# Optimization experiments

Measured on AMD Instinct MI355X. Metric: run time of the kernel, lower is better.

The kernel has to match this reference:

```python
import jax, jax.numpy as jnp
import numpy as np

B, S, E, H, D = 4, 2048, 1024, 16, 64


def setup_inputs() -> dict:
    key = jax.random.key(0)
    ks = jax.random.split(key, 10)
    s_in = 1.0 / np.sqrt(E)
    s_out = 1.0 / np.sqrt(H * D)
    return {
        "x": jax.random.normal(ks[0], (B, S, E), dtype=jnp.float32),
        "wq": jax.random.uniform(ks[1], (H, E, D), jnp.float32, -s_in, s_in),
        "bq": jax.random.uniform(ks[2], (H, D), jnp.float32, -s_in, s_in),
        "wk": jax.random.uniform(ks[3], (H, E, D), jnp.float32, -s_in, s_in),
        "bk": jax.random.uniform(ks[4], (H, D), jnp.float32, -s_in, s_in),
        "wv": jax.random.uniform(ks[5], (H, E, D), jnp.float32, -s_in, s_in),
        "bv": jax.random.uniform(ks[6], (H, D), jnp.float32, -s_in, s_in),
        "wo": jax.random.uniform(ks[7], (H * D, E), jnp.float32, -s_out, s_out),
        "bo": jax.random.uniform(ks[8], (E,), jnp.float32, -s_out, s_out),
    }


def reference(x, wq, bq, wk, bk, wv, bv, wo, bo):
    # Batched equivalent of the per-head Python loop: project all heads at once.
    q = jnp.einsum("bse,hed->bhsd", x, wq) + bq[None, :, None, :]
    k = jnp.einsum("bse,hed->bhsd", x, wk) + bk[None, :, None, :]
    v = jnp.einsum("bse,hed->bhsd", x, wv) + bv[None, :, None, :]
    scale = 1.0 / jnp.sqrt(jnp.asarray(D, dtype=x.dtype))
    scores = jnp.einsum("bhsd,bhtd->bhst", q, k) * scale  # [B,H,S,S]
    causal = jnp.tril(jnp.ones((S, S), dtype=bool))
    scores = jnp.where(causal[None, None], scores, jnp.asarray(-jnp.inf, x.dtype))
    p = jax.nn.softmax(scores, axis=-1)
    o = jnp.einsum("bhst,bhtd->bhsd", p, v)
    # concat heads along last dim (head order matches the torch cat order)
    o = jnp.transpose(o, (0, 2, 1, 3)).reshape(B, S, H * D)
    y = o @ wo + bo  # output projection; dropout is identity in eval
    return y
```

## Files before the change

### kernel.cpp

```cpp
#include <hip/hip_runtime.h>
#include <math.h>

#define B_ 4
#define S_ 2048
#define E_ 1024
#define H_ 16
#define D_ 64

using f32x4 = __attribute__((ext_vector_type(4))) float;
using s16x8 = __attribute__((ext_vector_type(8))) short;

__device__ __forceinline__ unsigned short f2bf(float f) {
    unsigned int u = __float_as_uint(f);
    u = (u + 0x7FFFu + ((u >> 16) & 1u)) >> 16;
    return (unsigned short)u;
}

__device__ __forceinline__ void load_lds16(const void* g, void* l) {
    __builtin_amdgcn_global_load_lds(
        (const __attribute__((address_space(1))) void*)g,
        (__attribute__((address_space(3))) void*)l, 16, 0, 0);
}

#define QSCALE 0.18033688011112042f

__global__ __launch_bounds__(256)
void cast_x(const float* __restrict__ in, unsigned short* __restrict__ out)
{
    const size_t idx = (size_t)blockIdx.x * 2048 + threadIdx.x * 8;
    const float4 v0 = *(const float4*)&in[idx];
    const float4 v1 = *(const float4*)&in[idx + 4];
    uint4 p;
    p.x = (unsigned)f2bf(v0.x) | ((unsigned)f2bf(v0.y) << 16);
    p.y = (unsigned)f2bf(v0.z) | ((unsigned)f2bf(v0.w) << 16);
    p.z = (unsigned)f2bf(v1.x) | ((unsigned)f2bf(v1.y) << 16);
    p.w = (unsigned)f2bf(v1.z) | ((unsigned)f2bf(v1.w) << 16);
    *(uint4*)&out[idx] = p;
}

__global__ __launch_bounds__(256)
void transpose_w(const float* __restrict__ wq, const float* __restrict__ wk,
                 const float* __restrict__ wv, const float* __restrict__ wo,
                 unsigned short* __restrict__ Wqkvt, unsigned short* __restrict__ Wot)
{
    __shared__ float T[64][68];
    const int z = blockIdx.z;
    const float* in;
    unsigned short* out;
    int inStride, r0, c0;
    if (z < 48) {
        if (blockIdx.y != 0) return;
        const int t = z >> 4, h = z & 15;
        const float* W = (t == 0) ? wq : ((t == 1) ? wk : wv);
        in = W + (size_t)h * (E_ * D_);
        inStride = 64;
        out = Wqkvt + (size_t)(t * 1024 + h * 64) * 1024;
        r0 = blockIdx.x * 64; c0 = 0;
    } else {
        in = wo; inStride = 1024;
        out = Wot;
        r0 = blockIdx.x * 64; c0 = blockIdx.y * 64;
    }
    const int tid = threadIdx.x;
    #pragma unroll
    for (int i = 0; i < 4; ++i) {
        const int e = tid + i * 256;
        const int row = e >> 4, c4 = e & 15;
        const float4 v = *(const float4*)&in[(size_t)(r0 + row) * inStride + c0 + c4 * 4];
        T[row][c4 * 4 + 0] = v.x; T[row][c4 * 4 + 1] = v.y;
        T[row][c4 * 4 + 2] = v.z; T[row][c4 * 4 + 3] = v.w;
    }
    __syncthreads();
    #pragma unroll
    for (int i = 0; i < 2; ++i) {
        const int e = tid + i * 256;
        const int c = e >> 3, ch = e & 7;
        unsigned short h8[8];
        #pragma unroll
        for (int j = 0; j < 8; ++j) h8[j] = f2bf(T[ch * 8 + j][c]);
        uint4 p;
        p.x = (unsigned)h8[0] | ((unsigned)h8[1] << 16);
        p.y = (unsigned)h8[2] | ((unsigned)h8[3] << 16);
        p.z = (unsigned)h8[4] | ((unsigned)h8[5] << 16);
        p.w = (unsigned)h8[6] | ((unsigned)h8[7] << 16);
        *(uint4*)&out[(size_t)(c0 + c) * 1024 + r0 + ch * 8] = p;
    }
}

template<int MODE>
__global__ __launch_bounds__(256)
void gemm_mfma(const unsigned short* __restrict__ A,
               const unsigned short* __restrict__ Bt,
               const float* __restrict__ bq, const float* __restrict__ bk,
               const float* __restrict__ bv, const float* __restrict__ bo,
               unsigned short* __restrict__ Qb, unsigned short* __restrict__ Kb,
               unsigned short* __restrict__ Vt, float* __restrict__ Cout)
{
    __shared__ short As[128 * 64];
    __shared__ short Bs[128 * 64];

    const int tid  = threadIdx.x;
    const int w    = tid >> 6, lane = tid & 63;
    const int g    = lane >> 4, l15 = lane & 15;
    const int wm   = w >> 1, wn = w & 1;
    const int mbase = blockIdx.x * 128;
    const int nbase = blockIdx.y * 128;

    const int srow8 = lane >> 3;
    const int pswz  = (lane & 7) ^ srow8;

    f32x4 acc[4][4];
    #pragma unroll
    for (int mt = 0; mt < 4; ++mt)
        #pragma unroll
        for (int nt = 0; nt < 4; ++nt)
            acc[mt][nt] = (f32x4){0.f, 0.f, 0.f, 0.f};

    for (int k0 = 0; k0 < 1024; k0 += 64) {
        __syncthreads();
        #pragma unroll
        for (int c = 0; c < 4; ++c) {
            const int R = w * 32 + c * 8;
            const int grow = R + srow8;
            load_lds16(&A[(size_t)(mbase + grow) * 1024 + k0 + pswz * 8], &As[R * 64]);
            load_lds16(&Bt[(size_t)(nbase + grow) * 1024 + k0 + pswz * 8], &Bs[R * 64]);
        }
        __syncthreads();
        #pragma unroll
        for (int ks = 0; ks < 2; ++ks) {
            const int qa = ((g + ks * 4) ^ (l15 & 7)) * 8;
            s16x8 af[4], bf[4];
            #pragma unroll
            for (int mt = 0; mt < 4; ++mt)
                af[mt] = *(const s16x8*)&As[(wm * 64 + mt * 16 + l15) * 64 + qa];
            #pragma unroll
            for (int nt = 0; nt < 4; ++nt)
                bf[nt] = *(const s16x8*)&Bs[(wn * 64 + nt * 16 + l15) * 64 + qa];
            #pragma unroll
            for (int mt = 0; mt < 4; ++mt)
                #pragma unroll
                for (int nt = 0; nt < 4; ++nt)
                    acc[mt][nt] = __builtin_amdgcn_mfma_f32_16x16x32_bf16(
                        af[mt], bf[nt], acc[mt][nt], 0, 0, 0);
        }
    }

    #pragma unroll
    for (int nt = 0; nt < 4; ++nt) {
        const int ncol = nbase + wn * 64 + nt * 16 + l15;
        if (MODE == 0) {
            const int t  = ncol >> 10;
            const int hh = (ncol >> 6) & 15;
            const int d  = ncol & 63;
            const float* bias = (t == 0) ? bq : ((t == 1) ? bk : bv);
            const float sc = (t == 0) ? QSCALE : 1.0f;
            const float bval = bias[hh * 64 + d];
            #pragma unroll
            for (int mt = 0; mt < 4; ++mt)
                #pragma unroll
                for (int r = 0; r < 4; ++r) {
                    const int m = mbase + wm * 64 + mt * 16 + g * 4 + r;
                    const int b = m >> 11, s = m & 2047;
                    const unsigned short val = f2bf((acc[mt][nt][r] + bval) * sc);
                    if (t == 2)
                        Vt[((size_t)(b * 16 + hh) * 64 + d) * 2048 + s] = val;
                    else {
                        unsigned short* Out = (t == 0) ? Qb : Kb;
                        Out[((size_t)(b * 16 + hh) * 2048 + s) * 64 + d] = val;
                    }
                }
        } else {
            const float bval = bo[ncol];
            #pragma unroll
            for (int mt = 0; mt < 4; ++mt)
                #pragma unroll
                for (int r = 0; r < 4; ++r) {
                    const int m = mbase + wm * 64 + mt * 16 + g * 4 + r;
                    Cout[(size_t)m * 1024 + ncol] = acc[mt][nt][r] + bval;
                }
        }
    }
}

#define LDK 72
__global__ __launch_bounds__(512, 4)
void attn_mfma(const unsigned short* __restrict__ Qb,
               const unsigned short* __restrict__ Kb,
               const unsigned short* __restrict__ Vt,
               unsigned short* __restrict__ O)
{
    __shared__ short Kls[2][64 * LDK];
    __shared__ short Vls[2][64 * LDK];
    __shared__ short Pls[8][16 * LDK];

    const int tid  = threadIdx.x;
    const int w    = tid >> 6;
    const int lane = tid & 63;
    const int g    = lane >> 4;
    const int mrow = lane & 15;
    const int j    = blockIdx.x;
    const int j2   = 15 - j;
    const int h    = blockIdx.y;
    const int b    = blockIdx.z;

    const size_t hb = (size_t)(b * 16 + h) * (2048 * 64);
    const int qH = j2 * 128 + w * 16;
    const int qL = j * 128 + w * 16;

    s16x8 aqH[2], aqL[2];
    {
        const int rh = qH + mrow, rl = qL + mrow;
        aqH[0] = *(const s16x8*)&Qb[hb + (size_t)rh * 64 + g * 8];
        aqH[1] = *(const s16x8*)&Qb[hb + (size_t)rh * 64 + 32 + g * 8];
        aqL[0] = *(const s16x8*)&Qb[hb + (size_t)rl * 64 + g * 8];
        aqL[1] = *(const s16x8*)&Qb[hb + (size_t)rl * 64 + 32 + g * 8];
    }

    float lH[4] = {0.f, 0.f, 0.f, 0.f};
    float lL[4] = {0.f, 0.f, 0.f, 0.f};
    f32x4 OH[4], OL[4];
    #pragma unroll
    for (int nt = 0; nt < 4; ++nt) { OH[nt] = (f32x4){0.f,0.f,0.f,0.f}; OL[nt] = (f32x4){0.f,0.f,0.f,0.f}; }

    const int stages      = 32 - 2 * j;
    const int lightStages = 2 * j + 2;

    const int srow = tid >> 3, spart = tid & 7;
    uint4 kreg = *(const uint4*)&Kb[hb + (size_t)srow * 64 + spart * 8];
    uint4 vreg = *(const uint4*)&Vt[hb + (size_t)srow * 2048 + spart * 8];

    for (int t = 0; t < stages; ++t) {
        const int t0  = t * 64;
        const int buf = t & 1;
        *(uint4*)&Kls[buf][srow * LDK + spart * 8] = kreg;
        *(uint4*)&Vls[buf][srow * LDK + spart * 8] = vreg;
        if (t + 1 < stages) {
            kreg = *(const uint4*)&Kb[hb + (size_t)(t0 + 64 + srow) * 64 + spart * 8];
            vreg = *(const uint4*)&Vt[hb + (size_t)srow * 2048 + t0 + 64 + spart * 8];
        }
        __syncthreads();

        {
            f32x4 Sf[4];
            #pragma unroll
            for (int ct = 0; ct < 4; ++ct) {
                f32x4 acc = (f32x4){0.f, 0.f, 0.f, 0.f};
                const s16x8 bk0 = *(const s16x8*)&Kls[buf][(ct * 16 + mrow) * LDK + g * 8];
                const s16x8 bk1 = *(const s16x8*)&Kls[buf][(ct * 16 + mrow) * LDK + 32 + g * 8];
                acc = __builtin_amdgcn_mfma_f32_16x16x32_bf16(aqH[0], bk0, acc, 0, 0, 0);
                acc = __builtin_amdgcn_mfma_f32_16x16x32_bf16(aqH[1], bk1, acc, 0, 0, 0);
                Sf[ct] = acc;
            }
            const int rbase = qH + g * 4;
            if (t0 + 63 > qH) {
                #pragma unroll
                for (int ct = 0; ct < 4; ++ct) {
                    const int key = t0 + ct * 16 + mrow;
                    #pragma unroll
                    for (int r = 0; r < 4; ++r)
                        if (key > rbase + r) Sf[ct][r] = -1e30f;
                }
            }
            #pragma unroll
            for (int ct = 0; ct < 4; ++ct)
                #pragma unroll
                for (int r = 0; r < 4; ++r)
                    Sf[ct][r] = exp2f(Sf[ct][r]);
            #pragma unroll
            for (int r = 0; r < 4; ++r)
                lH[r] += (Sf[0][r] + Sf[1][r]) + (Sf[2][r] + Sf[3][r]);
            #pragma unroll
            for (int ct = 0; ct < 4; ++ct)
                #pragma unroll
                for (int r = 0; r < 4; ++r)
                    Pls[w][(g * 4 + r) * LDK + ct * 16 + mrow] = (short)f2bf(Sf[ct][r]);
            const s16x8 ap0 = *(const s16x8*)&Pls[w][mrow * LDK + g * 8];
            const s16x8 ap1 = *(const s16x8*)&Pls[w][mrow * LDK + 32 + g * 8];
            #pragma unroll
            for (int nt = 0; nt < 4; ++nt) {
                const s16x8 bv0 = *(const s16x8*)&Vls[buf][(nt * 16 + mrow) * LDK + g * 8];
                const s16x8 bv1 = *(const s16x8*)&Vls[buf][(nt * 16 + mrow) * LDK + 32 + g * 8];
                OH[nt] = __builtin_amdgcn_mfma_f32_16x16x32_bf16(ap0, bv0, OH[nt], 0, 0, 0);
                OH[nt] = __builtin_amdgcn_mfma_f32_16x16x32_bf16(ap1, bv1, OH[nt], 0, 0, 0);
            }
        }

        if (t < lightStages) {
            f32x4 Sf[4];
            #pragma unroll
            for (int ct = 0; ct < 4; ++ct) {
                f32x4 acc = (f32x4){0.f, 0.f, 0.f, 0.f};
                const s16x8 bk0 = *(const s16x8*)&Kls[buf][(ct * 16 + mrow) * LDK + g * 8];
                const s16x8 bk1 = *(const s16x8*)&Kls[buf][(ct * 16 + mrow) * LDK + 32 + g * 8];
                acc = __builtin_amdgcn_mfma_f32_16x16x32_bf16(aqL[0], bk0, acc, 0, 0, 0);
                acc = __builtin_amdgcn_mfma_f32_16x16x32_bf16(aqL[1], bk1, acc, 0, 0, 0);
                Sf[ct] = acc;
            }
            const int rbase = qL + g * 4;
            if (t0 + 63 > qL) {
                #pragma unroll
                for (int ct = 0; ct < 4; ++ct) {
                    const int key = t0 + ct * 16 + mrow;
                    #pragma unroll
                    for (int r = 0; r < 4; ++r)
                        if (key > rbase + r) Sf[ct][r] = -1e30f;
                }
            }
            #pragma unroll
            for (int ct = 0; ct < 4; ++ct)
                #pragma unroll
                for (int r = 0; r < 4; ++r)
                    Sf[ct][r] = exp2f(Sf[ct][r]);
            #pragma unroll
            for (int r = 0; r < 4; ++r)
                lL[r] += (Sf[0][r] + Sf[1][r]) + (Sf[2][r] + Sf[3][r]);
            #pragma unroll
            for (int ct = 0; ct < 4; ++ct)
                #pragma unroll
                for (int r = 0; r < 4; ++r)
                    Pls[w][(g * 4 + r) * LDK + ct * 16 + mrow] = (short)f2bf(Sf[ct][r]);
            const s16x8 ap0 = *(const s16x8*)&Pls[w][mrow * LDK + g * 8];
            const s16x8 ap1 = *(const s16x8*)&Pls[w][mrow * LDK + 32 + g * 8];
            #pragma unroll
            for (int nt = 0; nt < 4; ++nt) {
                const s16x8 bv0 = *(const s16x8*)&Vls[buf][(nt * 16 + mrow) * LDK + g * 8];
                const s16x8 bv1 = *(const s16x8*)&Vls[buf][(nt * 16 + mrow) * LDK + 32 + g * 8];
                OL[nt] = __builtin_amdgcn_mfma_f32_16x16x32_bf16(ap0, bv0, OL[nt], 0, 0, 0);
                OL[nt] = __builtin_amdgcn_mfma_f32_16x16x32_bf16(ap1, bv1, OL[nt], 0, 0, 0);
            }
        }
    }

    #pragma unroll
    for (int r = 0; r < 4; ++r) {
        lH[r] += __shfl_xor(lH[r], 1);
        lH[r] += __shfl_xor(lH[r], 2);
        lH[r] += __shfl_xor(lH[r], 4);
        lH[r] += __shfl_xor(lH[r], 8);
        lL[r] += __shfl_xor(lL[r], 1);
        lL[r] += __shfl_xor(lL[r], 2);
        lL[r] += __shfl_xor(lL[r], 4);
        lL[r] += __shfl_xor(lL[r], 8);
    }
    #pragma unroll
    for (int r = 0; r < 4; ++r) {
        const float invH = 1.0f / lH[r];
        const float invL = 1.0f / lL[r];
        const int rowH = qH + g * 4 + r;
        const int rowL = qL + g * 4 + r;
        #pragma unroll
        for (int nt = 0; nt < 4; ++nt) {
            O[(size_t)(b * 2048 + rowH) * 1024 + h * 64 + nt * 16 + mrow] =
                f2bf(OH[nt][r] * invH);
            O[(size_t)(b * 2048 + rowL) * 1024 + h * 64 + nt * 16 + mrow] =
                f2bf(OL[nt][r] * invL);
        }
    }
}

extern "C" void kernel_launch(void* const* d_in, const int* in_sizes, int n_in,
                              void* d_out, int out_size, void* d_ws, size_t ws_size,
                              hipStream_t stream) {
    const float* x  = (const float*)d_in[0];
    const float* wq = (const float*)d_in[1];
    const float* bq = (const float*)d_in[2];
    const float* wk = (const float*)d_in[3];
    const float* bk = (const float*)d_in[4];
    const float* wv = (const float*)d_in[5];
    const float* bv = (const float*)d_in[6];
    const float* wo = (const float*)d_in[7];
    const float* bo = (const float*)d_in[8];
    float* out = (float*)d_out;

    const size_t hsz = (size_t)B_ * H_ * S_ * D_;
    unsigned short* xb    = (unsigned short*)d_ws;
    unsigned short* Wqkvt = xb + hsz;
    unsigned short* Wot   = Wqkvt + (size_t)3072 * 1024;
    unsigned short* Qb    = Wot + (size_t)1024 * 1024;
    unsigned short* Kb    = Qb + hsz;
    unsigned short* Vt    = Kb + hsz;
    unsigned short* Ob    = Vt + hsz;

    cast_x<<<4096, 256, 0, stream>>>(x, xb);
    transpose_w<<<dim3(16, 16, 49), 256, 0, stream>>>(wq, wk, wv, wo, Wqkvt, Wot);
    gemm_mfma<0><<<dim3(64, 24), 256, 0, stream>>>(
        xb, Wqkvt, bq, bk, bv, nullptr, Qb, Kb, Vt, nullptr);
    attn_mfma<<<dim3(8, H_, B_), 512, 0, stream>>>(Qb, Kb, Vt, Ob);
    gemm_mfma<1><<<dim3(64, 8), 256, 0, stream>>>(
        Ob, Wot, nullptr, nullptr, nullptr, bo, nullptr, nullptr, nullptr, out);
}
```

Before: 279.4 us.

## Transpose attention MFMA layout and route P through ds_bpermute instead of LDS

The QK^T and PV MFMAs are swapped to compute transposed tiles (K as A operand, Q as B), so each lane holds one query's scores. The P tile then goes from the score layout to the PV operand layout through ds_bpermute shuffles instead of a per-wave LDS write/read round trip. This drops the Pls shared buffer, which shrinks LDS use. It also packs bf16 with a cheaper round-half-up perm, simplifies the row-sum reduction, and stores the output as 8-byte vectors. The tradeoffs are 16 bpermutes and selects per half-tile, and bf16 rounding that differs slightly from round-to-nearest-even.

```diff
diff --git a/kernel.cpp b/kernel.cpp
--- a/kernel.cpp
+++ b/kernel.cpp
@@ -14,6 +14,12 @@
     unsigned int u = __float_as_uint(f);
     u = (u + 0x7FFFu + ((u >> 16) & 1u)) >> 16;
     return (unsigned short)u;
+}
+
+__device__ __forceinline__ unsigned int pack_bf2(float lo, float hi) {
+    const unsigned int ulo = __float_as_uint(lo) + 0x8000u;
+    const unsigned int uhi = __float_as_uint(hi) + 0x8000u;
+    return __builtin_amdgcn_perm(uhi, ulo, 0x07060302u);
 }
 
 __device__ __forceinline__ void load_lds16(const void* g, void* l) {
@@ -191,13 +197,12 @@
 {
     __shared__ short Kls[2][64 * LDK];
     __shared__ short Vls[2][64 * LDK];
-    __shared__ short Pls[8][16 * LDK];
 
     const int tid  = threadIdx.x;
     const int w    = tid >> 6;
     const int lane = tid & 63;
     const int g    = lane >> 4;
-    const int mrow = lane & 15;
+    const int l15  = lane & 15;
     const int j    = blockIdx.x;
     const int j2   = 15 - j;
     const int h    = blockIdx.y;
@@ -209,15 +214,14 @@
 
     s16x8 aqH[2], aqL[2];
     {
-        const int rh = qH + mrow, rl = qL + mrow;
+        const int rh = qH + l15, rl = qL + l15;
         aqH[0] = *(const s16x8*)&Qb[hb + (size_t)rh * 64 + g * 8];
         aqH[1] = *(const s16x8*)&Qb[hb + (size_t)rh * 64 + 32 + g * 8];
         aqL[0] = *(const s16x8*)&Qb[hb + (size_t)rl * 64 + g * 8];
         aqL[1] = *(const s16x8*)&Qb[hb + (size_t)rl * 64 + 32 + g * 8];
     }
 
-    float lH[4] = {0.f, 0.f, 0.f, 0.f};
-    float lL[4] = {0.f, 0.f, 0.f, 0.f};
+    float lsumH = 0.f, lsumL = 0.f;
     f32x4 OH[4], OL[4];
     #pragma unroll
     for (int nt = 0; nt < 4; ++nt) { OH[nt] = (f32x4){0.f,0.f,0.f,0.f}; OL[nt] = (f32x4){0.f,0.f,0.f,0.f}; }
@@ -228,6 +232,9 @@
     const int srow = tid >> 3, spart = tid & 7;
     uint4 kreg = *(const uint4*)&Kb[hb + (size_t)srow * 64 + spart * 8];
     uint4 vreg = *(const uint4*)&Vt[hb + (size_t)srow * 2048 + spart * 8];
+
+    const int addrA = (32 * (g & 1) + l15) * 4;
+    const int addrB = addrA + 64;
 
     for (int t = 0; t < stages; ++t) {
         const int t0  = t * 64;
@@ -240,120 +247,99 @@
         }
         __syncthreads();
 
-        {
+        #pragma unroll
+        for (int half = 0; half < 2; ++half) {
+            if (half == 1 && t >= lightStages) break;
+            const s16x8* aq   = (half == 0) ? aqH : aqL;
+            const int qbase   = (half == 0) ? qH : qL;
+
             f32x4 Sf[4];
             #pragma unroll
             for (int ct = 0; ct < 4; ++ct) {
                 f32x4 acc = (f32x4){0.f, 0.f, 0.f, 0.f};
-                const s16x8 bk0 = *(const s16x8*)&Kls[buf][(ct * 16 + mrow) * LDK + g * 8];
-                const s16x8 bk1 = *(const s16x8*)&Kls[buf][(ct * 16 + mrow) * LDK + 32 + g * 8];
-                acc = __builtin_amdgcn_mfma_f32_16x16x32_bf16(aqH[0], bk0, acc, 0, 0, 0);
-                acc = __builtin_amdgcn_mfma_f32_16x16x32_bf16(aqH[1], bk1, acc, 0, 0, 0);
+                const s16x8 bk0 = *(const s16x8*)&Kls[buf][(ct * 16 + l15) * LDK + g * 8];
+                const s16x8 bk1 = *(const s16x8*)&Kls[buf][(ct * 16 + l15) * LDK + 32 + g * 8];
+                acc = __builtin_amdgcn_mfma_f32_16x16x32_bf16(bk0, aq[0], acc, 0, 0, 0);
+                acc = __builtin_amdgcn_mfma_f32_16x16x32_bf16(bk1, aq[1], acc, 0, 0, 0);
                 Sf[ct] = acc;
             }
-            const int rbase = qH + g * 4;
-            if (t0 + 63 > qH) {
+
+            if (t0 + 63 > qbase) {
+                const int query = qbase + l15;
                 #pragma unroll
                 for (int ct = 0; ct < 4; ++ct) {
-                    const int key = t0 + ct * 16 + mrow;
+                    const int kbase = t0 + ct * 16 + g * 4;
                     #pragma unroll
                     for (int r = 0; r < 4; ++r)
-                        if (key > rbase + r) Sf[ct][r] = -1e30f;
+                        if (kbase + r > query) Sf[ct][r] = -1e30f;
                 }
             }
-            #pragma unroll
-            for (int ct = 0; ct < 4; ++ct)
-                #pragma unroll
-                for (int r = 0; r < 4; ++r)
-                    Sf[ct][r] = exp2f(Sf[ct][r]);
-            #pragma unroll
-            for (int r = 0; r < 4; ++r)
-                lH[r] += (Sf[0][r] + Sf[1][r]) + (Sf[2][r] + Sf[3][r]);
-            #pragma unroll
-            for (int ct = 0; ct < 4; ++ct)
-                #pragma unroll
-                for (int r = 0; r < 4; ++r)
-                    Pls[w][(g * 4 + r) * LDK + ct * 16 + mrow] = (short)f2bf(Sf[ct][r]);
-            const s16x8 ap0 = *(const s16x8*)&Pls[w][mrow * LDK + g * 8];
-            const s16x8 ap1 = *(const s16x8*)&Pls[w][mrow * LDK + 32 + g * 8];
+
+            float lacc = 0.f;
+            #pragma unroll
+            for (int ct = 0; ct < 4; ++ct) {
+                #pragma unroll
+                for (int r = 0; r < 4; ++r) Sf[ct][r] = exp2f(Sf[ct][r]);
+                lacc += (Sf[ct][0] + Sf[ct][1]) + (Sf[ct][2] + Sf[ct][3]);
+            }
+            if (half == 0) lsumH += lacc; else lsumL += lacc;
+
+            unsigned int P01[4], P23[4];
+            #pragma unroll
+            for (int ct = 0; ct < 4; ++ct) {
+                P01[ct] = pack_bf2(Sf[ct][0], Sf[ct][1]);
+                P23[ct] = pack_bf2(Sf[ct][2], Sf[ct][3]);
+            }
+
+            s16x8 Bf[2];
+            #pragma unroll
+            for (int kh = 0; kh < 2; ++kh) {
+                const int c0 = kh * 2, c1 = kh * 2 + 1;
+                union { int i[4]; s16x8 v; } u;
+                const int a0 = __builtin_amdgcn_ds_bpermute(addrA, (int)P01[c0]);
+                const int a1 = __builtin_amdgcn_ds_bpermute(addrA, (int)P01[c1]);
+                u.i[0] = (g < 2) ? a0 : a1;
+                const int b0 = __builtin_amdgcn_ds_bpermute(addrA, (int)P23[c0]);
+                const int b1 = __builtin_amdgcn_ds_bpermute(addrA, (int)P23[c1]);
+                u.i[1] = (g < 2) ? b0 : b1;
+                const int c0v = __builtin_amdgcn_ds_bpermute(addrB, (int)P01[c0]);
+                const int c1v = __builtin_amdgcn_ds_bpermute(addrB, (int)P01[c1]);
+                u.i[2] = (g < 2) ? c0v : c1v;
+                const int d0 = __builtin_amdgcn_ds_bpermute(addrB, (int)P23[c0]);
+                const int d1 = __builtin_amdgcn_ds_bpermute(addrB, (int)P23[c1]);
+                u.i[3] = (g < 2) ? d0 : d1;
+                Bf[kh] = u.v;
+            }
+
+            f32x4* Oacc = (half == 0) ? OH : OL;
             #pragma unroll
             for (int nt = 0; nt < 4; ++nt) {
-                const s16x8 bv0 = *(const s16x8*)&Vls[buf][(nt * 16 + mrow) * LDK + g * 8];
-                const s16x8 bv1 = *(const s16x8*)&Vls[buf][(nt * 16 + mrow) * LDK + 32 + g * 8];
-                OH[nt] = __builtin_amdgcn_mfma_f32_16x16x32_bf16(ap0, bv0, OH[nt], 0, 0, 0);
-                OH[nt] = __builtin_amdgcn_mfma_f32_16x16x32_bf16(ap1, bv1, OH[nt], 0, 0, 0);
-            }
-        }
-
-        if (t < lightStages) {
-            f32x4 Sf[4];
-            #pragma unroll
-            for (int ct = 0; ct < 4; ++ct) {
-                f32x4 acc = (f32x4){0.f, 0.f, 0.f, 0.f};
-                const s16x8 bk0 = *(const s16x8*)&Kls[buf][(ct * 16 + mrow) * LDK + g * 8];
-                const s16x8 bk1 = *(const s16x8*)&Kls[buf][(ct * 16 + mrow) * LDK + 32 + g * 8];
-                acc = __builtin_amdgcn_mfma_f32_16x16x32_bf16(aqL[0], bk0, acc, 0, 0, 0);
-                acc = __builtin_amdgcn_mfma_f32_16x16x32_bf16(aqL[1], bk1, acc, 0, 0, 0);
-                Sf[ct] = acc;
-            }
-            const int rbase = qL + g * 4;
-            if (t0 + 63 > qL) {
-                #pragma unroll
-                for (int ct = 0; ct < 4; ++ct) {
-                    const int key = t0 + ct * 16 + mrow;
-                    #pragma unroll
-                    for (int r = 0; r < 4; ++r)
-                        if (key > rbase + r) Sf[ct][r] = -1e30f;
-                }
-            }
-            #pragma unroll
-            for (int ct = 0; ct < 4; ++ct)
-                #pragma unroll
-                for (int r = 0; r < 4; ++r)
-                    Sf[ct][r] = exp2f(Sf[ct][r]);
-            #pragma unroll
-            for (int r = 0; r < 4; ++r)
-                lL[r] += (Sf[0][r] + Sf[1][r]) + (Sf[2][r] + Sf[3][r]);
-            #pragma unroll
-            for (int ct = 0; ct < 4; ++ct)
-                #pragma unroll
-                for (int r = 0; r < 4; ++r)
-                    Pls[w][(g * 4 + r) * LDK + ct * 16 + mrow] = (short)f2bf(Sf[ct][r]);
-            const s16x8 ap0 = *(const s16x8*)&Pls[w][mrow * LDK + g * 8];
-            const s16x8 ap1 = *(const s16x8*)&Pls[w][mrow * LDK + 32 + g * 8];
-            #pragma unroll
-            for (int nt = 0; nt < 4; ++nt) {
-                const s16x8 bv0 = *(const s16x8*)&Vls[buf][(nt * 16 + mrow) * LDK + g * 8];
-                const s16x8 bv1 = *(const s16x8*)&Vls[buf][(nt * 16 + mrow) * LDK + 32 + g * 8];
-                OL[nt] = __builtin_amdgcn_mfma_f32_16x16x32_bf16(ap0, bv0, OL[nt], 0, 0, 0);
-                OL[nt] = __builtin_amdgcn_mfma_f32_16x16x32_bf16(ap1, bv1, OL[nt], 0, 0, 0);
-            }
-        }
-    }
-
-    #pragma unroll
-    for (int r = 0; r < 4; ++r) {
-        lH[r] += __shfl_xor(lH[r], 1);
-        lH[r] += __shfl_xor(lH[r], 2);
-        lH[r] += __shfl_xor(lH[r], 4);
-        lH[r] += __shfl_xor(lH[r], 8);
-        lL[r] += __shfl_xor(lL[r], 1);
-        lL[r] += __shfl_xor(lL[r], 2);
-        lL[r] += __shfl_xor(lL[r], 4);
-        lL[r] += __shfl_xor(lL[r], 8);
-    }
-    #pragma unroll
-    for (int r = 0; r < 4; ++r) {
-        const float invH = 1.0f / lH[r];
-        const float invL = 1.0f / lL[r];
-        const int rowH = qH + g * 4 + r;
-        const int rowL = qL + g * 4 + r;
+                const s16x8 bv0 = *(const s16x8*)&Vls[buf][(nt * 16 + l15) * LDK + g * 8];
+                const s16x8 bv1 = *(const s16x8*)&Vls[buf][(nt * 16 + l15) * LDK + 32 + g * 8];
+                Oacc[nt] = __builtin_amdgcn_mfma_f32_16x16x32_bf16(bv0, Bf[0], Oacc[nt], 0, 0, 0);
+                Oacc[nt] = __builtin_amdgcn_mfma_f32_16x16x32_bf16(bv1, Bf[1], Oacc[nt], 0, 0, 0);
+            }
+        }
+    }
+
+    lsumH += __shfl_xor(lsumH, 16);
+    lsumH += __shfl_xor(lsumH, 32);
+    lsumL += __shfl_xor(lsumL, 16);
+    lsumL += __shfl_xor(lsumL, 32);
+    const float invH = 1.0f / lsumH;
+    const float invL = 1.0f / lsumL;
+
+    #pragma unroll
+    for (int half = 0; half < 2; ++half) {
+        const f32x4* Oacc = (half == 0) ? OH : OL;
+        const float  inv  = (half == 0) ? invH : invL;
+        const int query   = ((half == 0) ? qH : qL) + l15;
         #pragma unroll
         for (int nt = 0; nt < 4; ++nt) {
-            O[(size_t)(b * 2048 + rowH) * 1024 + h * 64 + nt * 16 + mrow] =
-                f2bf(OH[nt][r] * invH);
-            O[(size_t)(b * 2048 + rowL) * 1024 + h * 64 + nt * 16 + mrow] =
-                f2bf(OL[nt][r] * invL);
+            const unsigned int lo = pack_bf2(Oacc[nt][0] * inv, Oacc[nt][1] * inv);
+            const unsigned int hi = pack_bf2(Oacc[nt][2] * inv, Oacc[nt][3] * inv);
+            uint2 pk; pk.x = lo; pk.y = hi;
+            *(uint2*)&O[(size_t)(b * 2048 + query) * 1024 + h * 64 + nt * 16 + g * 4] = pk;
         }
     }
 }
```

Measured after the change: 283.6 us. No clear change (+1.5%).
